# Kernel tuning notes

Measured on AMD Instinct MI355X. Metric: run time of the kernel, lower is better.

The kernel has to match this reference:

```python
import jax, jax.numpy as jnp
import numpy as np

EPS = 1e-7  # keras backend epsilon


def setup_inputs() -> dict:
    key = jax.random.key(0)
    k1, k2, k3, k4 = jax.random.split(key, 4)
    B, S, D = 32, 2048, 1024
    x = jax.random.normal(k1, (B, S, D), dtype=jnp.float32)
    y = jax.random.normal(k2, (B, D), dtype=jnp.float32)
    mask = jax.random.randint(k3, (B, S), 0, 2, dtype=jnp.int32)
    # glorot-uniform-ish init for M (d_x, d_y)
    limit = float(np.sqrt(6.0 / (D + D)))
    M = jax.random.uniform(k4, (D, D), dtype=jnp.float32, minval=-limit, maxval=limit)
    return {"x": x, "y": y, "mask": mask, "M": M}


def reference(x, y, mask, M):
    # (M @ y^T)^T == y @ M^T  -> [B, d_x]
    proj = jnp.einsum('bd,ed->be', y, M)
    # broadcast over steps instead of materializing the repeat: [B, S]
    eij = jnp.tanh(jnp.einsum('bsd,bd->bs', x, proj))
    a = jnp.exp(eij) * mask.astype(x.dtype)
    a = a / (jnp.sum(a, axis=1, keepdims=True) + EPS)
    return a
```

## Files before the change

### kernel.cpp

```cpp
#include <hip/hip_runtime.h>
#include <math.h>

#define BB 32
#define SS 2048
#define DD 1024
#define EPSF 1e-7f

__global__ __launch_bounds__(256) void proj_kernel(const float* __restrict__ y,
                                                   const float* __restrict__ M,
                                                   float* __restrict__ proj) {
    const int wave = (blockIdx.x * 256 + threadIdx.x) >> 6;
    const int lane = threadIdx.x & 63;
    const int b = wave >> 10;
    const int e = wave & 1023;

    const float4* __restrict__ Mrow = (const float4*)(M + (size_t)e * DD);
    const float4* __restrict__ yrow = (const float4*)(y + (size_t)b * DD);

    float acc = 0.f;
#pragma unroll
    for (int k = 0; k < 4; ++k) {
        const int idx = lane + 64 * k;
        const float4 m  = Mrow[idx];
        const float4 yy = yrow[idx];
        acc += m.x * yy.x + m.y * yy.y + m.z * yy.z + m.w * yy.w;
    }
#pragma unroll
    for (int off = 32; off >= 1; off >>= 1)
        acc += __shfl_xor(acc, off, 64);

    if (lane == 0) proj[wave] = acc;
}

__global__ __launch_bounds__(256) void score_kernel(const float* __restrict__ x,
                                                    const int* __restrict__ mask,
                                                    const float* __restrict__ proj,
                                                    float* __restrict__ t) {
    const int wave = (blockIdx.x * 256 + threadIdx.x) >> 6;
    const int lane = threadIdx.x & 63;
    const int b = wave >> 11;
    const int s = wave & 2047;

    const int m = mask[(size_t)b * SS + s];
    if (m == 0) {
        if (lane == 0) t[(size_t)b * SS + s] = 0.f;
        return;
    }

    const float4* __restrict__ xr = (const float4*)(x + ((size_t)b * SS + s) * DD);
    const float4* __restrict__ pr = (const float4*)(proj + (size_t)b * DD);

    float acc = 0.f;
#pragma unroll
    for (int k = 0; k < 4; ++k) {
        const int idx = lane + 64 * k;
        const float4 xv = xr[idx];
        const float4 pv = pr[idx];
        acc += xv.x * pv.x + xv.y * pv.y + xv.z * pv.z + xv.w * pv.w;
    }
#pragma unroll
    for (int off = 32; off >= 1; off >>= 1)
        acc += __shfl_xor(acc, off, 64);

    if (lane == 0) t[(size_t)b * SS + s] = expf(tanhf(acc));
}

__global__ __launch_bounds__(256) void norm_kernel(float* __restrict__ out) {
    const int b = blockIdx.x;
    float* __restrict__ row = out + (size_t)b * SS;

    float vals[8];
    float sum = 0.f;
#pragma unroll
    for (int k = 0; k < 8; ++k) {
        vals[k] = row[threadIdx.x + 256 * k];
        sum += vals[k];
    }
#pragma unroll
    for (int off = 32; off >= 1; off >>= 1)
        sum += __shfl_xor(sum, off, 64);

    __shared__ float wsum[4];
    const int lane = threadIdx.x & 63;
    const int wid  = threadIdx.x >> 6;
    if (lane == 0) wsum[wid] = sum;
    __syncthreads();
    const float total = wsum[0] + wsum[1] + wsum[2] + wsum[3];
    const float inv = 1.0f / (total + EPSF);

#pragma unroll
    for (int k = 0; k < 8; ++k)
        row[threadIdx.x + 256 * k] = vals[k] * inv;
}

extern "C" void kernel_launch(void* const* d_in, const int* in_sizes, int n_in,
                              void* d_out, int out_size, void* d_ws, size_t ws_size,
                              hipStream_t stream) {
    const float* x    = (const float*)d_in[0];
    const float* y    = (const float*)d_in[1];
    const int*   mask = (const int*)d_in[2];
    const float* M    = (const float*)d_in[3];
    float* out  = (float*)d_out;
    float* proj = (float*)d_ws;

    proj_kernel<<<(BB * DD) / 4, 256, 0, stream>>>(y, M, proj);
    score_kernel<<<(BB * SS) / 4, 256, 0, stream>>>(x, mask, proj, out);
    norm_kernel<<<BB, 256, 0, stream>>>(out);
}
```

Measured before the change: 343.7 us.

## Reuse M rows across batches in proj and process two rows per wave in score

The projection kernel now stages 16 batch rows of y in shared memory and has each wave keep one M row in registers while looping over those 16 batches. M is therefore read from global memory twice instead of once per batch. The score kernel handles two sequence positions per wave, loads proj once for both, reads the mask as an int2, and uses nontemporal loads for x. The aim is less redundant traffic and more memory-level parallelism, at the cost of fewer waves for the projection and 64KB of LDS per block.

Measured after the change: 327.3 us. 1.05x faster.

```diff
diff --git a/kernel.cpp b/kernel.cpp
--- a/kernel.cpp
+++ b/kernel.cpp
@@ -6,30 +6,45 @@
 #define DD 1024
 #define EPSF 1e-7f
 
+typedef float vfloat4 __attribute__((ext_vector_type(4)));
+
 __global__ __launch_bounds__(256) void proj_kernel(const float* __restrict__ y,
                                                    const float* __restrict__ M,
                                                    float* __restrict__ proj) {
-    const int wave = (blockIdx.x * 256 + threadIdx.x) >> 6;
-    const int lane = threadIdx.x & 63;
-    const int b = wave >> 10;
-    const int e = wave & 1023;
+    __shared__ vfloat4 yl[16 * 256];
+    const int eg  = blockIdx.x >> 1;
+    const int bh  = blockIdx.x & 1;
+    const int tid = threadIdx.x;
 
-    const float4* __restrict__ Mrow = (const float4*)(M + (size_t)e * DD);
-    const float4* __restrict__ yrow = (const float4*)(y + (size_t)b * DD);
+    const vfloat4* __restrict__ ysrc = (const vfloat4*)(y + (size_t)bh * 16 * DD);
+#pragma unroll
+    for (int k = 0; k < 16; ++k)
+        yl[tid + 256 * k] = ysrc[tid + 256 * k];
+    __syncthreads();
 
-    float acc = 0.f;
+    const int wave = tid >> 6;
+    const int lane = tid & 63;
+    const int e = eg * 4 + wave;
+
+    const vfloat4* __restrict__ Mrow = (const vfloat4*)(M + (size_t)e * DD);
+    vfloat4 m[4];
 #pragma unroll
-    for (int k = 0; k < 4; ++k) {
-        const int idx = lane + 64 * k;
-        const float4 m  = Mrow[idx];
-        const float4 yy = yrow[idx];
-        acc += m.x * yy.x + m.y * yy.y + m.z * yy.z + m.w * yy.w;
+    for (int k = 0; k < 4; ++k)
+        m[k] = Mrow[lane + 64 * k];
+
+    for (int b = 0; b < 16; ++b) {
+        float acc = 0.f;
+#pragma unroll
+        for (int k = 0; k < 4; ++k) {
+            const vfloat4 yv = yl[b * 256 + lane + 64 * k];
+            acc += m[k].x * yv.x + m[k].y * yv.y + m[k].z * yv.z + m[k].w * yv.w;
+        }
+#pragma unroll
+        for (int off = 32; off >= 1; off >>= 1)
+            acc += __shfl_xor(acc, off, 64);
+        if (lane == 0)
+            proj[(size_t)(bh * 16 + b) * DD + e] = acc;
     }
-#pragma unroll
-    for (int off = 32; off >= 1; off >>= 1)
-        acc += __shfl_xor(acc, off, 64);
-
-    if (lane == 0) proj[wave] = acc;
 }
 
 __global__ __launch_bounds__(256) void score_kernel(const float* __restrict__ x,
@@ -38,31 +53,49 @@
                                                     float* __restrict__ t) {
     const int wave = (blockIdx.x * 256 + threadIdx.x) >> 6;
     const int lane = threadIdx.x & 63;
-    const int b = wave >> 11;
-    const int s = wave & 2047;
+    const int b  = wave >> 10;
+    const int s0 = (wave & 1023) << 1;
+    const size_t base = (size_t)b * SS + s0;
 
-    const int m = mask[(size_t)b * SS + s];
-    if (m == 0) {
-        if (lane == 0) t[(size_t)b * SS + s] = 0.f;
+    const int2 mm = *(const int2*)(mask + base);
+    if ((mm.x | mm.y) == 0) {
+        if (lane == 0) { t[base] = 0.f; t[base + 1] = 0.f; }
         return;
     }
 
-    const float4* __restrict__ xr = (const float4*)(x + ((size_t)b * SS + s) * DD);
-    const float4* __restrict__ pr = (const float4*)(proj + (size_t)b * DD);
+    const vfloat4* __restrict__ pr = (const vfloat4*)(proj + (size_t)b * DD);
+    vfloat4 p[4];
+#pragma unroll
+    for (int k = 0; k < 4; ++k)
+        p[k] = pr[lane + 64 * k];
 
-    float acc = 0.f;
+    const vfloat4* __restrict__ x0 = (const vfloat4*)(x + base * (size_t)DD);
+    const vfloat4* __restrict__ x1 = x0 + 256;
+
+    float acc0 = 0.f, acc1 = 0.f;
+    if (mm.x) {
 #pragma unroll
-    for (int k = 0; k < 4; ++k) {
-        const int idx = lane + 64 * k;
-        const float4 xv = xr[idx];
-        const float4 pv = pr[idx];
-        acc += xv.x * pv.x + xv.y * pv.y + xv.z * pv.z + xv.w * pv.w;
+        for (int k = 0; k < 4; ++k) {
+            const vfloat4 xv = __builtin_nontemporal_load(&x0[lane + 64 * k]);
+            acc0 += xv.x * p[k].x + xv.y * p[k].y + xv.z * p[k].z + xv.w * p[k].w;
+        }
+    }
+    if (mm.y) {
+#pragma unroll
+        for (int k = 0; k < 4; ++k) {
+            const vfloat4 xv = __builtin_nontemporal_load(&x1[lane + 64 * k]);
+            acc1 += xv.x * p[k].x + xv.y * p[k].y + xv.z * p[k].z + xv.w * p[k].w;
+        }
     }
 #pragma unroll
-    for (int off = 32; off >= 1; off >>= 1)
-        acc += __shfl_xor(acc, off, 64);
-
-    if (lane == 0) t[(size_t)b * SS + s] = expf(tanhf(acc));
+    for (int off = 32; off >= 1; off >>= 1) {
+        acc0 += __shfl_xor(acc0, off, 64);
+        acc1 += __shfl_xor(acc1, off, 64);
+    }
+    if (lane == 0) {
+        t[base]     = mm.x ? expf(tanhf(acc0)) : 0.f;
+        t[base + 1] = mm.y ? expf(tanhf(acc1)) : 0.f;
+    }
 }
 
 __global__ __launch_bounds__(256) void norm_kernel(float* __restrict__ out) {
@@ -103,7 +136,7 @@
     float* out  = (float*)d_out;
     float* proj = (float*)d_ws;
 
-    proj_kernel<<<(BB * DD) / 4, 256, 0, stream>>>(y, M, proj);
-    score_kernel<<<(BB * SS) / 4, 256, 0, stream>>>(x, mask, proj, out);
+    proj_kernel<<<512, 256, 0, stream>>>(y, M, proj);
+    score_kernel<<<(BB * SS / 2) / 4, 256, 0, stream>>>(x, mask, proj, out);
     norm_kernel<<<BB, 256, 0, stream>>>(out);
 }
```
